# Optimization experiments

Measured on AMD Instinct MI355X. Metric: run time of the kernel, lower is better.

Reference implementation:

```python
import jax, jax.numpy as jnp
import numpy as np

BN_EPS = 1e-5
NUM_ROUTING_ITERS = 3


def _bn(x, gamma, beta, axes):
    # training-mode batch norm (torch default train mode): batch statistics
    mean = x.mean(axes, keepdims=True)
    var = x.var(axes, keepdims=True)
    return (x - mean) * jax.lax.rsqrt(var + BN_EPS) * gamma + beta


def _squash(x):
    # squash over last dim: sn * x / ((1+sn) * sqrt(sn))
    sn = jnp.sum(x * x, axis=-1, keepdims=True)
    return sn * x / ((1.0 + sn) * jnp.sqrt(sn))


def setup_inputs() -> dict:
    key = jax.random.key(0)
    ks = jax.random.split(key, 16)
    B, N = 4, 2048          # batch, num_points
    P, Q = 1024, 16         # prim_caps_size, prim_vec_size
    L, V = 64, 64           # latent_caps_size, latent_vec_size
    OUT = 40
    s = 0.02
    return {
        "x": jax.random.normal(ks[0], (B, 3, N), dtype=jnp.float32),
        # ConvLayer
        "w1": jax.random.normal(ks[1], (64, 3), dtype=jnp.float32) * s,
        "b1": jnp.zeros((64,), jnp.float32),
        "g1": jnp.ones((64,), jnp.float32),
        "be1": jnp.zeros((64,), jnp.float32),
        "w2": jax.random.normal(ks[2], (128, 64), dtype=jnp.float32) * s,
        "b2": jnp.zeros((128,), jnp.float32),
        "g2": jnp.ones((128,), jnp.float32),
        "be2": jnp.zeros((128,), jnp.float32),
        # PrimaryPointCapsLayer: Q parallel conv1d(128->P, k=1)+BN branches, stacked
        "w3": jax.random.normal(ks[3], (Q, P, 128), dtype=jnp.float32) * s,
        "b3": jnp.zeros((Q, P), jnp.float32),
        "g3": jnp.ones((Q, P), jnp.float32),
        "be3": jnp.zeros((Q, P), jnp.float32),
        # LatentCapsLayer routing weights
        "Wr": jax.random.normal(ks[4], (L, P, V, Q), dtype=jnp.float32) * 0.01,
        # classifier head
        "fc_w": jax.random.normal(ks[5], (OUT, L * V), dtype=jnp.float32) * s,
        "fc_b": jnp.zeros((OUT,), jnp.float32),
    }


def reference(x, w1, b1, g1, be1, w2, b2, g2, be2, w3, b3, g3, be3, Wr, fc_w, fc_b):
    B = x.shape[0]
    # ConvLayer: two 1x1 conv1d + BN + ReLU
    h = jnp.einsum("oc,bcn->bon", w1, x) + b1[None, :, None]
    h = jax.nn.relu(_bn(h, g1[None, :, None], be1[None, :, None], (0, 2)))
    h = jnp.einsum("oc,bcn->bon", w2, h) + b2[None, :, None]
    h = jax.nn.relu(_bn(h, g2[None, :, None], be2[None, :, None], (0, 2)))  # [B,128,N]

    # PrimaryPointCapsLayer: Q branches of conv1d+BN+global maxpool, vectorized
    u = jnp.einsum("qpc,bcn->bqpn", w3, h) + b3[None, :, :, None]  # [B,Q,P,N]
    u = _bn(u, g3[None, :, :, None], be3[None, :, :, None], (0, 3))
    u = u.max(axis=-1)                      # global maxpool -> [B,Q,P]
    u = jnp.transpose(u, (0, 2, 1))         # stack dim=2 in torch -> [B,P,Q]
    u = _squash(u)                          # squash over prim_vec

    # LatentCapsLayer dynamic routing
    u_hat = jnp.einsum("lpvq,bpq->blpv", Wr, u)   # [B,L,P,V]
    u_hat_d = jax.lax.stop_gradient(u_hat)
    L, P = Wr.shape[0], Wr.shape[1]
    b_ij = jnp.zeros((B, L, P), u_hat.dtype)
    for _ in range(NUM_ROUTING_ITERS - 1):
        c_ij = jax.nn.softmax(b_ij, axis=1)
        v_j = _squash(jnp.einsum("blp,blpv->blv", c_ij, u_hat_d))
        b_ij = b_ij + jnp.einsum("blv,blpv->blp", v_j, u_hat_d)
    c_ij = jax.nn.softmax(b_ij, axis=1)
    v_j = _squash(jnp.einsum("blp,blpv->blv", c_ij, u_hat))  # [B,L,V]

    presence = jnp.linalg.norm(v_j, axis=2)                   # [B,L]
    logits = v_j.reshape(B, -1) @ fc_w.T + fc_b               # [B,OUT]
    return (logits, presence)
```

## Files before the change

### kernel.cpp

```cpp
#include <hip/hip_runtime.h>
#include <math.h>

#define BN_EPS 1e-5f

typedef __attribute__((ext_vector_type(8))) _Float16 half8;
typedef __attribute__((ext_vector_type(4))) float f32x4;
#define SPLIT_S  2048.0f
#define INV_S    (1.0f/2048.0f)

__global__ __launch_bounds__(256) void k_conv1stats(const float* __restrict__ x,
        const float* __restrict__ w1, float* __restrict__ y1,
        float* __restrict__ mean, float* __restrict__ inv) {
    const int o = blockIdx.x, t = threadIdx.x;
    const float wa = w1[o*3+0], wb = w1[o*3+1], wc = w1[o*3+2];
    float s = 0.f, ss = 0.f;
#pragma unroll
    for (int it = 0; it < 8; ++it) {
        int i = it * 256 + t;
        int b = i >> 9, n4 = (i & 511) * 4;
        const float* xb = x + (size_t)b * 6144 + n4;
        float4 x0 = *(const float4*)(xb);
        float4 x1 = *(const float4*)(xb + 2048);
        float4 x2 = *(const float4*)(xb + 4096);
        float4 r;
        r.x = wa*x0.x + wb*x1.x + wc*x2.x;
        r.y = wa*x0.y + wb*x1.y + wc*x2.y;
        r.z = wa*x0.z + wb*x1.z + wc*x2.z;
        r.w = wa*x0.w + wb*x1.w + wc*x2.w;
        *(float4*)(y1 + o * 8192 + i * 4) = r;
        s += r.x + r.y + r.z + r.w;
        ss = fmaf(r.x, r.x, fmaf(r.y, r.y, fmaf(r.z, r.z, fmaf(r.w, r.w, ss))));
    }
    __shared__ float rs[256], rss[256];
    rs[t] = s; rss[t] = ss;
    __syncthreads();
    for (int off = 128; off > 0; off >>= 1) {
        if (t < off) { rs[t] += rs[t+off]; rss[t] += rss[t+off]; }
        __syncthreads();
    }
    if (t == 0) {
        float m = rs[0] * (1.f/8192.f);
        float var = rss[0] * (1.f/8192.f) - m*m;
        mean[o] = m;
        inv[o]  = rsqrtf(var + BN_EPS);
    }
}

__global__ void k_stats(const float* __restrict__ y, float* __restrict__ mean,
                        float* __restrict__ inv) {
    int c = blockIdx.x, t = threadIdx.x;
    float s = 0.f, ss = 0.f;
    const float4* src = (const float4*)(y + c * 8192);
    for (int i = t; i < 2048; i += 256) {
        float4 v = src[i];
        s += v.x + v.y + v.z + v.w;
        ss = fmaf(v.x, v.x, fmaf(v.y, v.y, fmaf(v.z, v.z, fmaf(v.w, v.w, ss))));
    }
    __shared__ float rs[256], rss[256];
    rs[t] = s; rss[t] = ss;
    __syncthreads();
    for (int off = 128; off > 0; off >>= 1) {
        if (t < off) { rs[t] += rs[t+off]; rss[t] += rss[t+off]; }
        __syncthreads();
    }
    if (t == 0) {
        float m = rs[0] * (1.f/8192.f);
        float var = rss[0] * (1.f/8192.f) - m*m;
        mean[c] = m;
        inv[c]  = rsqrtf(var + BN_EPS);
    }
}

__global__ __launch_bounds__(256) void k_conv2(const float* __restrict__ y1,
        const float* __restrict__ w2,
        const float* __restrict__ mean1, const float* __restrict__ inv1,
        const float* __restrict__ g1, const float* __restrict__ be1,
        float* __restrict__ y2) {
    __shared__ float sc1[64], sh1[64];
    const int t = threadIdx.x;
    if (t < 64) {
        float sc = inv1[t] * g1[t];
        sc1[t] = sc;
        sh1[t] = be1[t] - mean1[t] * sc;
    }
    __syncthreads();
    int bn0 = (blockIdx.x * 256 + t) * 4;
    int og0 = blockIdx.y * 4;
    float4 acc[4];
#pragma unroll
    for (int j = 0; j < 4; ++j) acc[j] = float4{0.f,0.f,0.f,0.f};
    for (int c = 0; c < 64; ++c) {
        float4 hv = *(const float4*)(y1 + c*8192 + bn0);
        float sc = sc1[c], sh = sh1[c];
        hv.x = fmaxf(fmaf(hv.x, sc, sh), 0.f);
        hv.y = fmaxf(fmaf(hv.y, sc, sh), 0.f);
        hv.z = fmaxf(fmaf(hv.z, sc, sh), 0.f);
        hv.w = fmaxf(fmaf(hv.w, sc, sh), 0.f);
#pragma unroll
        for (int j = 0; j < 4; ++j) {
            float w = w2[(og0+j)*64 + c];
            acc[j].x = fmaf(w, hv.x, acc[j].x); acc[j].y = fmaf(w, hv.y, acc[j].y);
            acc[j].z = fmaf(w, hv.z, acc[j].z); acc[j].w = fmaf(w, hv.w, acc[j].w);
        }
    }
#pragma unroll
    for (int j = 0; j < 4; ++j) *(float4*)(y2 + (og0+j)*8192 + bn0) = acc[j];
}

__global__ void k_split_w3(const float* __restrict__ w, _Float16* __restrict__ hi,
                           _Float16* __restrict__ lo) {
    int base = blockIdx.x * 256 + threadIdx.x;
#pragma unroll
    for (int it = 0; it < 4; ++it) {
        int i = (base + it * 131072) * 4;
        float4 d = *reinterpret_cast<const float4*>(w + i);
        float vs[4] = {d.x, d.y, d.z, d.w};
#pragma unroll
        for (int j = 0; j < 4; ++j) {
            _Float16 h = (_Float16)vs[j];
            hi[i + j] = h;
            lo[i + j] = (_Float16)((vs[j] - (float)h) * SPLIT_S);
        }
    }
}

__global__ __launch_bounds__(256) void k_h2t_split(const float* __restrict__ y2,
        const float* __restrict__ mean, const float* __restrict__ inv,
        const float* __restrict__ g, const float* __restrict__ be,
        _Float16* __restrict__ hi, _Float16* __restrict__ lo) {
    __shared__ float tile[64][65];
    const int t = threadIdx.x;
    const int bn0 = blockIdx.x * 64, c0 = blockIdx.y * 64;
#pragma unroll
    for (int r = 0; r < 16; ++r) {
        int idx = r * 256 + t;
        int cl = idx >> 6, bnl = idx & 63;
        int c = c0 + cl;
        float v = y2[(size_t)c * 8192 + bn0 + bnl];
        v = (v - mean[c]) * inv[c] * g[c] + be[c];
        tile[cl][bnl] = v > 0.f ? v : 0.f;
    }
    __syncthreads();
#pragma unroll
    for (int r = 0; r < 16; ++r) {
        int idx = r * 256 + t;
        int bnl = idx >> 6, cl = idx & 63;
        float v = tile[cl][bnl];
        _Float16 h = (_Float16)v;
        size_t o = (size_t)(bn0 + bnl) * 128 + c0 + cl;
        hi[o] = h;
        lo[o] = (_Float16)((v - (float)h) * SPLIT_S);
    }
}

__global__ __launch_bounds__(256, 2) void k_caps(
        const _Float16* __restrict__ w3h, const _Float16* __restrict__ w3l,
        const _Float16* __restrict__ h2h, const _Float16* __restrict__ h2l,
        float* __restrict__ umax, float* __restrict__ umin,
        float* __restrict__ usum_b, float* __restrict__ usumsq_b) {
    const int lane = threadIdx.x & 63, wave = threadIdx.x >> 6;
    const int b = blockIdx.y;
    const int mrow = blockIdx.x * 128 + wave * 32;
    const int r16 = lane & 15, kq = lane >> 4;

    __shared__ _Float16 Bs[2][2][8][64][8];

    half8 Ah[2][4], Al[2][4];
#pragma unroll
    for (int mt = 0; mt < 2; ++mt) {
        const size_t base = (size_t)(mrow + mt*16 + r16) * 128 + kq * 8;
#pragma unroll
        for (int ks = 0; ks < 4; ++ks) {
            Ah[mt][ks] = *reinterpret_cast<const half8*>(w3h + base + ks*32);
            Al[mt][ks] = *reinterpret_cast<const half8*>(w3l + base + ks*32);
        }
    }
    float mx[2][4], mn[2][4], sm[2][4], sq[2][4];
#pragma unroll
    for (int mt = 0; mt < 2; ++mt)
#pragma unroll
        for (int r = 0; r < 4; ++r) {
            mx[mt][r] = -3.4e38f; mn[mt][r] = 3.4e38f; sm[mt][r] = 0.f; sq[mt][r] = 0.f;
        }

    const int u0 = wave * 2;
    const size_t srow = (size_t)(b*2048 + r16) * 128 + wave * 32 + kq * 8;

    {
#pragma unroll
        for (int g = 0; g < 2; ++g) {
            const size_t a = srow + (size_t)g * 16 * 128;
            *reinterpret_cast<half8*>(&Bs[0][g][u0  ][lane][0]) = *reinterpret_cast<const half8*>(h2h + a);
            *reinterpret_cast<half8*>(&Bs[0][g][u0+1][lane][0]) = *reinterpret_cast<const half8*>(h2l + a);
        }
    }
    __syncthreads();

    for (int nt = 0; nt < 64; ++nt) {
        const int buf = nt & 1;
        const int ntn = (nt + 1 < 64) ? nt + 1 : nt;
        const size_t snext = srow + (size_t)ntn * 32 * 128;
        half8 g0h = *reinterpret_cast<const half8*>(h2h + snext);
        half8 g0l = *reinterpret_cast<const half8*>(h2l + snext);
        half8 g1h = *reinterpret_cast<const half8*>(h2h + snext + 2048);
        half8 g1l = *reinterpret_cast<const half8*>(h2l + snext + 2048);

#pragma unroll
        for (int g = 0; g < 2; ++g) {
            f32x4 acc[2], accx[2];
#pragma unroll
            for (int mt = 0; mt < 2; ++mt) { acc[mt] = f32x4{0.f,0.f,0.f,0.f}; accx[mt] = f32x4{0.f,0.f,0.f,0.f}; }
#pragma unroll
            for (int ks = 0; ks < 4; ++ks) {
                half8 Bh = *reinterpret_cast<const half8*>(&Bs[buf][g][ks*2  ][lane][0]);
                half8 Bl = *reinterpret_cast<const half8*>(&Bs[buf][g][ks*2+1][lane][0]);
#pragma unroll
                for (int mt = 0; mt < 2; ++mt) {
                    acc[mt]  = __builtin_amdgcn_mfma_f32_16x16x32_f16(Ah[mt][ks], Bh, acc[mt], 0, 0, 0);
                    accx[mt] = __builtin_amdgcn_mfma_f32_16x16x32_f16(Ah[mt][ks], Bl, accx[mt], 0, 0, 0);
                    accx[mt] = __builtin_amdgcn_mfma_f32_16x16x32_f16(Al[mt][ks], Bh, accx[mt], 0, 0, 0);
                }
            }
#pragma unroll
            for (int mt = 0; mt < 2; ++mt)
#pragma unroll
                for (int r = 0; r < 4; ++r) {
                    float v = fmaf(accx[mt][r], INV_S, acc[mt][r]);
                    mx[mt][r] = fmaxf(mx[mt][r], v);
                    mn[mt][r] = fminf(mn[mt][r], v);
                    sm[mt][r] += v;
                    sq[mt][r] = fmaf(v, v, sq[mt][r]);
                }
        }
        *reinterpret_cast<half8*>(&Bs[buf^1][0][u0  ][lane][0]) = g0h;
        *reinterpret_cast<half8*>(&Bs[buf^1][0][u0+1][lane][0]) = g0l;
        *reinterpret_cast<half8*>(&Bs[buf^1][1][u0  ][lane][0]) = g1h;
        *reinterpret_cast<half8*>(&Bs[buf^1][1][u0+1][lane][0]) = g1l;
        __syncthreads();
    }

#pragma unroll
    for (int off = 8; off >= 1; off >>= 1)
#pragma unroll
        for (int mt = 0; mt < 2; ++mt)
#pragma unroll
            for (int r = 0; r < 4; ++r) {
                mx[mt][r] = fmaxf(mx[mt][r], __shfl_xor(mx[mt][r], off));
                mn[mt][r] = fminf(mn[mt][r], __shfl_xor(mn[mt][r], off));
                sm[mt][r] += __shfl_xor(sm[mt][r], off);
                sq[mt][r] += __shfl_xor(sq[mt][r], off);
            }
    if (r16 == 0) {
#pragma unroll
        for (int mt = 0; mt < 2; ++mt)
#pragma unroll
            for (int r = 0; r < 4; ++r) {
                int qp = mrow + mt*16 + kq*4 + r;
                umax[b*16384 + qp]     = mx[mt][r];
                umin[b*16384 + qp]     = mn[mt][r];
                usum_b[b*16384 + qp]   = sm[mt][r];
                usumsq_b[b*16384 + qp] = sq[mt][r];
            }
    }
}

__global__ void k_u(const float* __restrict__ umax, const float* __restrict__ umin,
                    const float* __restrict__ usum_b, const float* __restrict__ usumsq_b,
                    const float* __restrict__ g3, const float* __restrict__ be3,
                    float* __restrict__ u) {
    int tg = blockIdx.x * 256 + threadIdx.x;
    int b = tg >> 10, p = tg & 1023;
    float ub[16]; float sn = 0.f;
#pragma unroll
    for (int q = 0; q < 16; ++q) {
        int qp = q * 1024 + p;
        float s  = usum_b[qp] + usum_b[16384+qp] + usum_b[32768+qp] + usum_b[49152+qp];
        float ss = usumsq_b[qp] + usumsq_b[16384+qp] + usumsq_b[32768+qp] + usumsq_b[49152+qp];
        float mean  = s * (1.f/8192.f);
        float var   = ss * (1.f/8192.f) - mean*mean;
        float scale = g3[qp] * rsqrtf(var + BN_EPS);
        float val = (scale >= 0.f) ? umax[b*16384 + qp] : umin[b*16384 + qp];
        float vb = (val - mean) * scale + be3[qp];
        ub[q] = vb; sn = fmaf(vb, vb, sn);
    }
    float f = sqrtf(sn) / (1.f + sn);
#pragma unroll
    for (int q = 0; q < 16; ++q) u[tg*16 + q] = ub[q] * f;
}

__global__ __launch_bounds__(256) void k_uhat(const float* __restrict__ Wr,
                                              const float* __restrict__ u,
                                              float* __restrict__ uhat2,
                                              float* __restrict__ s1p) {
    const int t = threadIdx.x;
    const int pblk = blockIdx.x, l = blockIdx.y;
    __shared__ float wr[4][16][68];
    __shared__ float us[4][4][16];
    const int bb = t >> 6, v = t & 63;
    float s1acc = 0.f;
    for (int sub = 0; sub < 8; ++sub) {
        const int p0 = pblk * 32 + sub * 4;
        const float* src = Wr + ((size_t)l * 1024 + p0) * 1024;
        if (sub) __syncthreads();
#pragma unroll
        for (int it = 0; it < 4; ++it) {
            float4 d = *(const float4*)(src + (it*256 + t) * 4);
            int vv = t >> 2, q0 = (t & 3) * 4;
            wr[it][q0  ][vv] = d.x; wr[it][q0+1][vv] = d.y;
            wr[it][q0+2][vv] = d.z; wr[it][q0+3][vv] = d.w;
        }
        {
            int p = t >> 6, b2 = (t >> 4) & 3, q = t & 15;
            us[p][b2][q] = u[((size_t)b2 * 1024 + p0 + p) * 16 + q];
        }
        __syncthreads();
#pragma unroll
        for (int p = 0; p < 4; ++p) {
            float acc = 0.f;
#pragma unroll
            for (int q = 0; q < 16; ++q) acc = fmaf(wr[p][q][v], us[p][bb][q], acc);
            uhat2[(((size_t)bb * 1024 + p0 + p) * 64 + l) * 64 + v] = acc;
            s1acc += acc;
        }
    }
    s1p[(((size_t)pblk * 4 + bb) * 64 + l) * 64 + v] = s1acc;
}

__global__ void k_s1red(const float* __restrict__ s1p, float* __restrict__ vout) {
    const int wv = blockIdx.x;
    const int b = wv >> 6, l = wv & 63;
    const int v = threadIdx.x;
    float acc = 0.f;
#pragma unroll
    for (int pblk = 0; pblk < 32; ++pblk)
        acc += s1p[(((size_t)pblk * 4 + b) * 64 + l) * 64 + v];
    float s = acc * (1.f/64.f);
    float sn = s * s;
#pragma unroll
    for (int off = 32; off >= 1; off >>= 1) sn += __shfl_xor(sn, off);
    vout[wv * 64 + v] = s * sqrtf(sn) / (1.f + sn);
}

__global__ __launch_bounds__(256) void k_route(const float* __restrict__ uhat2,
                                               const float* __restrict__ vin,
                                               float* __restrict__ bij,
                                               float* __restrict__ part, const int read_b) {
    const int blk = blockIdx.x;
    const int b = blk >> 7, ch = blk & 127;
    const int p0 = ch * 8;
    const int t = threadIdx.x;
    const int v = t & 63, w = t >> 6;
    __shared__ float uh[64][68];
    __shared__ float vs[64][68];
    __shared__ float bl[64];
    __shared__ float cl[64];
    {
        const float* src = vin + b * 4096;
        for (int i = t; i < 1024; i += 256) {
            float4 d = *(const float4*)(src + i * 4);
            int l = i >> 4, v0 = (i & 15) * 4;
            vs[l][v0] = d.x; vs[l][v0+1] = d.y; vs[l][v0+2] = d.z; vs[l][v0+3] = d.w;
        }
    }
    float sacc[16];
#pragma unroll
    for (int j = 0; j < 16; ++j) sacc[j] = 0.f;

    for (int pp = 0; pp < 8; ++pp) {
        const int p = p0 + pp;
        __syncthreads();
        const float* src = uhat2 + ((size_t)b * 1024 + p) * 4096;
        for (int i = t; i < 1024; i += 256) {
            float4 d = *(const float4*)(src + i * 4);
            int l = i >> 4, v0 = (i & 15) * 4;
            uh[l][v0] = d.x; uh[l][v0+1] = d.y; uh[l][v0+2] = d.z; uh[l][v0+3] = d.w;
        }
        __syncthreads();
#pragma unroll
        for (int i = 0; i < 16; ++i) {
            const int l = w * 16 + i;
            float prod = uh[l][v] * vs[l][v];
#pragma unroll
            for (int off = 32; off >= 1; off >>= 1) prod += __shfl_xor(prod, off);
            if (v == 0) {
                float bb = prod;
                if (read_b) bb += bij[(b * 64 + l) * 1024 + p];
                bl[l] = bb;
                if (!read_b) bij[(b * 64 + l) * 1024 + p] = bb;
            }
        }
        __syncthreads();
        if (w == 0) {
            float xv = bl[v];
            float m = xv;
#pragma unroll
            for (int off = 32; off >= 1; off >>= 1) m = fmaxf(m, __shfl_xor(m, off));
            float e = expf(xv - m);
            float sgm = e;
#pragma unroll
            for (int off = 32; off >= 1; off >>= 1) sgm += __shfl_xor(sgm, off);
            cl[v] = e / sgm;
        }
        __syncthreads();
#pragma unroll
        for (int j = 0; j < 16; ++j) {
            const int l = j * 4 + w;
            sacc[j] = fmaf(cl[l], uh[l][v], sacc[j]);
        }
    }
#pragma unroll
    for (int j = 0; j < 16; ++j) {
        const int l = j * 4 + w;
        part[((size_t)(b * 128 + ch) * 64 + l) * 64 + v] = sacc[j];
    }
}

__global__ void k_red_squash(const float* __restrict__ part, float* __restrict__ vout,
                             float* __restrict__ pres) {
    const int wv = blockIdx.x;
    const int b = wv >> 6, l = wv & 63;
    const int v = threadIdx.x;
    float acc = 0.f;
    for (int ch = 0; ch < 128; ++ch) acc += part[((size_t)(b * 128 + ch) * 64 + l) * 64 + v];
    float sn = acc * acc;
#pragma unroll
    for (int off = 32; off >= 1; off >>= 1) sn += __shfl_xor(sn, off);
    vout[wv * 64 + v] = acc * sqrtf(sn) / (1.f + sn);
    if (pres != nullptr && v == 0) pres[wv] = sn / (1.f + sn);
}

__global__ void k_logits(const float* __restrict__ vj, const float* __restrict__ fcw,
                         const float* __restrict__ fcb, float* __restrict__ out) {
    int wv = blockIdx.x * 4 + (threadIdx.x >> 6);
    int lane = threadIdx.x & 63;
    int b = wv / 40, o = wv % 40;
    const float* xv = vj + b * 4096;
    const float* wr = fcw + (size_t)o * 4096;
    float acc = 0.f;
    for (int i = lane; i < 4096; i += 64) acc = fmaf(xv[i], wr[i], acc);
#pragma unroll
    for (int off = 32; off >= 1; off >>= 1) acc += __shfl_xor(acc, off);
    if (lane == 0) out[b * 40 + o] = acc + fcb[o];
}

extern "C" void kernel_launch(void* const* d_in, const int* in_sizes, int n_in,
                              void* d_out, int out_size, void* d_ws, size_t ws_size,
                              hipStream_t stream) {
    const float* x   = (const float*)d_in[0];
    const float* w1  = (const float*)d_in[1];
    const float* g1  = (const float*)d_in[3];
    const float* be1 = (const float*)d_in[4];
    const float* w2  = (const float*)d_in[5];
    const float* g2  = (const float*)d_in[7];
    const float* be2 = (const float*)d_in[8];
    const float* w3  = (const float*)d_in[9];
    const float* g3  = (const float*)d_in[11];
    const float* be3 = (const float*)d_in[12];
    const float* Wr  = (const float*)d_in[13];
    const float* fcw = (const float*)d_in[14];
    const float* fcb = (const float*)d_in[15];
    float* out = (float*)d_out;

    float* ws       = (float*)d_ws;
    float* y1       = ws;
    float* y2       = y1 + 524288;
    float* mean1    = y2 + 1048576;
    float* inv1     = mean1 + 64;
    float* mean2    = inv1 + 64;
    float* inv2     = mean2 + 128;
    float* umax     = inv2 + 128;
    float* umin     = umax + 65536;
    float* usum_b   = umin + 65536;
    float* usumsq_b = usum_b + 65536;
    float* u        = usumsq_b + 65536;
    float* v1       = u + 65536;
    float* v2       = v1 + 16384;
    float* vj       = v2 + 16384;
    float* bij      = vj + 16384;
    float* s1p      = bij + 262144;
    float* part     = s1p + 524288;
    float* uhat2    = part + 2097152;
    _Float16* w3h = (_Float16*)uhat2;
    _Float16* w3l = w3h + 2097152;
    _Float16* h2h = w3l + 2097152;
    _Float16* h2l = h2h + 1048576;

    k_conv1stats<<<64, 256, 0, stream>>>(x, w1, y1, mean1, inv1);
    k_conv2<<<dim3(8, 32), 256, 0, stream>>>(y1, w2, mean1, inv1, g1, be1, y2);
    k_stats<<<128, 256, 0, stream>>>(y2, mean2, inv2);
    k_split_w3<<<512, 256, 0, stream>>>(w3, w3h, w3l);
    k_h2t_split<<<dim3(128, 2), 256, 0, stream>>>(y2, mean2, inv2, g2, be2, h2h, h2l);
    k_caps<<<dim3(128, 4), 256, 0, stream>>>(w3h, w3l, h2h, h2l, umax, umin, usum_b, usumsq_b);
    k_u<<<16, 256, 0, stream>>>(umax, umin, usum_b, usumsq_b, g3, be3, u);
    k_uhat<<<dim3(32, 64), 256, 0, stream>>>(Wr, u, uhat2, s1p);
    k_s1red<<<256, 64, 0, stream>>>(s1p, v1);
    k_route<<<512, 256, 0, stream>>>(uhat2, v1, bij, part, 0);
    k_red_squash<<<256, 64, 0, stream>>>(part, v2, nullptr);
    k_route<<<512, 256, 0, stream>>>(uhat2, v2, bij, part, 1);
    k_red_squash<<<256, 64, 0, stream>>>(part, vj, out + 160);
    k_logits<<<40, 256, 0, stream>>>(vj, fcw, fcb, out);
}
```

Measured before the change: 694.0 us.

## Fold BN gamma sign into w3, drop min tracking, vectorize stores and softmax

```diff
diff --git a/kernel.cpp b/kernel.cpp
--- a/kernel.cpp
+++ b/kernel.cpp
@@ -4,6 +4,7 @@
 #define BN_EPS 1e-5f
 
 typedef __attribute__((ext_vector_type(8))) _Float16 half8;
+typedef __attribute__((ext_vector_type(4))) _Float16 half4;
 typedef __attribute__((ext_vector_type(4))) float f32x4;
 #define SPLIT_S  2048.0f
 #define INV_S    (1.0f/2048.0f)
@@ -107,20 +108,24 @@
     for (int j = 0; j < 4; ++j) *(float4*)(y2 + (og0+j)*8192 + bn0) = acc[j];
 }
 
-__global__ void k_split_w3(const float* __restrict__ w, _Float16* __restrict__ hi,
-                           _Float16* __restrict__ lo) {
+__global__ void k_split_w3(const float* __restrict__ w, const float* __restrict__ g3,
+                           _Float16* __restrict__ hi, _Float16* __restrict__ lo) {
     int base = blockIdx.x * 256 + threadIdx.x;
 #pragma unroll
     for (int it = 0; it < 4; ++it) {
         int i = (base + it * 131072) * 4;
         float4 d = *reinterpret_cast<const float4*>(w + i);
-        float vs[4] = {d.x, d.y, d.z, d.w};
+        float sgn = (g3[i >> 7] < 0.f) ? -1.f : 1.f;
+        float vs[4] = {d.x * sgn, d.y * sgn, d.z * sgn, d.w * sgn};
+        half4 h4, l4;
 #pragma unroll
         for (int j = 0; j < 4; ++j) {
             _Float16 h = (_Float16)vs[j];
-            hi[i + j] = h;
-            lo[i + j] = (_Float16)((vs[j] - (float)h) * SPLIT_S);
-        }
+            h4[j] = h;
+            l4[j] = (_Float16)((vs[j] - (float)h) * SPLIT_S);
+        }
+        *reinterpret_cast<half4*>(hi + i) = h4;
+        *reinterpret_cast<half4*>(lo + i) = l4;
     }
 }
 
@@ -132,31 +137,41 @@
     const int t = threadIdx.x;
     const int bn0 = blockIdx.x * 64, c0 = blockIdx.y * 64;
 #pragma unroll
-    for (int r = 0; r < 16; ++r) {
+    for (int r = 0; r < 4; ++r) {
         int idx = r * 256 + t;
-        int cl = idx >> 6, bnl = idx & 63;
+        int cl = idx >> 4, bn4 = (idx & 15) * 4;
         int c = c0 + cl;
-        float v = y2[(size_t)c * 8192 + bn0 + bnl];
-        v = (v - mean[c]) * inv[c] * g[c] + be[c];
-        tile[cl][bnl] = v > 0.f ? v : 0.f;
+        float sc = inv[c] * g[c];
+        float sh = be[c] - mean[c] * sc;
+        float4 d = *(const float4*)(y2 + (size_t)c * 8192 + bn0 + bn4);
+        tile[cl][bn4  ] = fmaxf(fmaf(d.x, sc, sh), 0.f);
+        tile[cl][bn4+1] = fmaxf(fmaf(d.y, sc, sh), 0.f);
+        tile[cl][bn4+2] = fmaxf(fmaf(d.z, sc, sh), 0.f);
+        tile[cl][bn4+3] = fmaxf(fmaf(d.w, sc, sh), 0.f);
     }
     __syncthreads();
 #pragma unroll
-    for (int r = 0; r < 16; ++r) {
+    for (int r = 0; r < 4; ++r) {
         int idx = r * 256 + t;
-        int bnl = idx >> 6, cl = idx & 63;
-        float v = tile[cl][bnl];
-        _Float16 h = (_Float16)v;
-        size_t o = (size_t)(bn0 + bnl) * 128 + c0 + cl;
-        hi[o] = h;
-        lo[o] = (_Float16)((v - (float)h) * SPLIT_S);
+        int bnl = idx >> 4, c4 = (idx & 15) * 4;
+        half4 h4, l4;
+#pragma unroll
+        for (int j = 0; j < 4; ++j) {
+            float v = tile[c4 + j][bnl];
+            _Float16 h = (_Float16)v;
+            h4[j] = h;
+            l4[j] = (_Float16)((v - (float)h) * SPLIT_S);
+        }
+        size_t o = (size_t)(bn0 + bnl) * 128 + c0 + c4;
+        *reinterpret_cast<half4*>(hi + o) = h4;
+        *reinterpret_cast<half4*>(lo + o) = l4;
     }
 }
 
 __global__ __launch_bounds__(256, 2) void k_caps(
         const _Float16* __restrict__ w3h, const _Float16* __restrict__ w3l,
         const _Float16* __restrict__ h2h, const _Float16* __restrict__ h2l,
-        float* __restrict__ umax, float* __restrict__ umin,
+        float* __restrict__ umax,
         float* __restrict__ usum_b, float* __restrict__ usumsq_b) {
     const int lane = threadIdx.x & 63, wave = threadIdx.x >> 6;
     const int b = blockIdx.y;
@@ -175,12 +190,12 @@
             Al[mt][ks] = *reinterpret_cast<const half8*>(w3l + base + ks*32);
         }
     }
-    float mx[2][4], mn[2][4], sm[2][4], sq[2][4];
+    float mx[2][4], sm[2][4], sq[2][4];
 #pragma unroll
     for (int mt = 0; mt < 2; ++mt)
 #pragma unroll
         for (int r = 0; r < 4; ++r) {
-            mx[mt][r] = -3.4e38f; mn[mt][r] = 3.4e38f; sm[mt][r] = 0.f; sq[mt][r] = 0.f;
+            mx[mt][r] = -3.4e38f; sm[mt][r] = 0.f; sq[mt][r] = 0.f;
         }
 
     const int u0 = wave * 2;
@@ -227,7 +242,6 @@
                 for (int r = 0; r < 4; ++r) {
                     float v = fmaf(accx[mt][r], INV_S, acc[mt][r]);
                     mx[mt][r] = fmaxf(mx[mt][r], v);
-                    mn[mt][r] = fminf(mn[mt][r], v);
                     sm[mt][r] += v;
                     sq[mt][r] = fmaf(v, v, sq[mt][r]);
                 }
@@ -246,7 +260,6 @@
 #pragma unroll
             for (int r = 0; r < 4; ++r) {
                 mx[mt][r] = fmaxf(mx[mt][r], __shfl_xor(mx[mt][r], off));
-                mn[mt][r] = fminf(mn[mt][r], __shfl_xor(mn[mt][r], off));
                 sm[mt][r] += __shfl_xor(sm[mt][r], off);
                 sq[mt][r] += __shfl_xor(sq[mt][r], off);
             }
@@ -257,14 +270,13 @@
             for (int r = 0; r < 4; ++r) {
                 int qp = mrow + mt*16 + kq*4 + r;
                 umax[b*16384 + qp]     = mx[mt][r];
-                umin[b*16384 + qp]     = mn[mt][r];
                 usum_b[b*16384 + qp]   = sm[mt][r];
                 usumsq_b[b*16384 + qp] = sq[mt][r];
             }
     }
 }
 
-__global__ void k_u(const float* __restrict__ umax, const float* __restrict__ umin,
+__global__ void k_u(const float* __restrict__ umax,
                     const float* __restrict__ usum_b, const float* __restrict__ usumsq_b,
                     const float* __restrict__ g3, const float* __restrict__ be3,
                     float* __restrict__ u) {
@@ -276,10 +288,12 @@
         int qp = q * 1024 + p;
         float s  = usum_b[qp] + usum_b[16384+qp] + usum_b[32768+qp] + usum_b[49152+qp];
         float ss = usumsq_b[qp] + usumsq_b[16384+qp] + usumsq_b[32768+qp] + usumsq_b[49152+qp];
-        float mean  = s * (1.f/8192.f);
+        float g  = g3[qp];
+        float sgn = (g < 0.f) ? -1.f : 1.f;
+        float mean  = sgn * s * (1.f/8192.f);
         float var   = ss * (1.f/8192.f) - mean*mean;
-        float scale = g3[qp] * rsqrtf(var + BN_EPS);
-        float val = (scale >= 0.f) ? umax[b*16384 + qp] : umin[b*16384 + qp];
+        float scale = g * rsqrtf(var + BN_EPS);
+        float val = sgn * umax[b*16384 + qp];
         float vb = (val - mean) * scale + be3[qp];
         ub[q] = vb; sn = fmaf(vb, vb, sn);
     }
@@ -294,7 +308,7 @@
                                               float* __restrict__ s1p) {
     const int t = threadIdx.x;
     const int pblk = blockIdx.x, l = blockIdx.y;
-    __shared__ float wr[4][16][68];
+    __shared__ float wr[4][64][20];
     __shared__ float us[4][4][16];
     const int bb = t >> 6, v = t & 63;
     float s1acc = 0.f;
@@ -306,8 +320,7 @@
         for (int it = 0; it < 4; ++it) {
             float4 d = *(const float4*)(src + (it*256 + t) * 4);
             int vv = t >> 2, q0 = (t & 3) * 4;
-            wr[it][q0  ][vv] = d.x; wr[it][q0+1][vv] = d.y;
-            wr[it][q0+2][vv] = d.z; wr[it][q0+3][vv] = d.w;
+            *(float4*)&wr[it][vv][q0] = d;
         }
         {
             int p = t >> 6, b2 = (t >> 4) & 3, q = t & 15;
@@ -318,7 +331,14 @@
         for (int p = 0; p < 4; ++p) {
             float acc = 0.f;
 #pragma unroll
-            for (int q = 0; q < 16; ++q) acc = fmaf(wr[p][q][v], us[p][bb][q], acc);
+            for (int q4 = 0; q4 < 4; ++q4) {
+                float4 wf = *(const float4*)&wr[p][v][q4*4];
+                float4 uf = *(const float4*)&us[p][bb][q4*4];
+                acc = fmaf(wf.x, uf.x, acc);
+                acc = fmaf(wf.y, uf.y, acc);
+                acc = fmaf(wf.z, uf.z, acc);
+                acc = fmaf(wf.w, uf.w, acc);
+            }
             uhat2[(((size_t)bb * 1024 + p0 + p) * 64 + l) * 64 + v] = acc;
             s1acc += acc;
         }
@@ -353,7 +373,6 @@
     __shared__ float uh[64][68];
     __shared__ float vs[64][68];
     __shared__ float bl[64];
-    __shared__ float cl[64];
     {
         const float* src = vin + b * 4096;
         for (int i = t; i < 1024; i += 256) {
@@ -390,22 +409,20 @@
             }
         }
         __syncthreads();
-        if (w == 0) {
-            float xv = bl[v];
-            float m = xv;
-#pragma unroll
-            for (int off = 32; off >= 1; off >>= 1) m = fmaxf(m, __shfl_xor(m, off));
-            float e = expf(xv - m);
-            float sgm = e;
-#pragma unroll
-            for (int off = 32; off >= 1; off >>= 1) sgm += __shfl_xor(sgm, off);
-            cl[v] = e / sgm;
-        }
-        __syncthreads();
+        float xv = bl[v];
+        float m = xv;
+#pragma unroll
+        for (int off = 32; off >= 1; off >>= 1) m = fmaxf(m, __shfl_xor(m, off));
+        float e = expf(xv - m);
+        float sgm = e;
+#pragma unroll
+        for (int off = 32; off >= 1; off >>= 1) sgm += __shfl_xor(sgm, off);
+        float c = e / sgm;
 #pragma unroll
         for (int j = 0; j < 16; ++j) {
             const int l = j * 4 + w;
-            sacc[j] = fmaf(cl[l], uh[l][v], sacc[j]);
+            float cl = __shfl(c, l);
+            sacc[j] = fmaf(cl, uh[l][v], sacc[j]);
         }
     }
 #pragma unroll
@@ -469,8 +486,7 @@
     float* mean2    = inv1 + 64;
     float* inv2     = mean2 + 128;
     float* umax     = inv2 + 128;
-    float* umin     = umax + 65536;
-    float* usum_b   = umin + 65536;
+    float* usum_b   = umax + 65536;
     float* usumsq_b = usum_b + 65536;
     float* u        = usumsq_b + 65536;
     float* v1       = u + 65536;
@@ -488,10 +504,10 @@
     k_conv1stats<<<64, 256, 0, stream>>>(x, w1, y1, mean1, inv1);
     k_conv2<<<dim3(8, 32), 256, 0, stream>>>(y1, w2, mean1, inv1, g1, be1, y2);
     k_stats<<<128, 256, 0, stream>>>(y2, mean2, inv2);
-    k_split_w3<<<512, 256, 0, stream>>>(w3, w3h, w3l);
+    k_split_w3<<<512, 256, 0, stream>>>(w3, g3, w3h, w3l);
     k_h2t_split<<<dim3(128, 2), 256, 0, stream>>>(y2, mean2, inv2, g2, be2, h2h, h2l);
-    k_caps<<<dim3(128, 4), 256, 0, stream>>>(w3h, w3l, h2h, h2l, umax, umin, usum_b, usumsq_b);
-    k_u<<<16, 256, 0, stream>>>(umax, umin, usum_b, usumsq_b, g3, be3, u);
+    k_caps<<<dim3(128, 4), 256, 0, stream>>>(w3h, w3l, h2h, h2l, umax, usum_b, usumsq_b);
+    k_u<<<16, 256, 0, stream>>>(umax, usum_b, usumsq_b, g3, be3, u);
     k_uhat<<<dim3(32, 64), 256, 0, stream>>>(Wr, u, uhat2, s1p);
     k_s1red<<<256, 64, 0, stream>>>(s1p, v1);
     k_route<<<512, 256, 0, stream>>>(uhat2, v1, bij, part, 0);
```

Measured after the change: 692.4 us. About the same (-0.2%).
